# Kernel tuning notes

Measured on AMD Instinct MI355X. Metric: run time of the kernel, lower is better.

## Reference

```python
import jax, jax.numpy as jnp
import numpy as np

N, D, B, E, H = 512, 32, 4, 256, 4
SEP = 256
HD = E // H


def setup_inputs() -> dict:
    key = jax.random.key(0)
    ks = jax.random.split(key, 8)
    s = 0.02
    return {
        "src": jax.random.normal(ks[0], (N, D, B, E), dtype=jnp.float32),
        "w_in_row": jax.random.normal(ks[1], (3 * E, E), dtype=jnp.float32) * s,
        "b_in_row": jnp.zeros((3 * E,), jnp.float32),
        "w_out_row": jax.random.normal(ks[2], (E, E), dtype=jnp.float32) * s,
        "b_out_row": jnp.zeros((E,), jnp.float32),
        "w_in_col": jax.random.normal(ks[3], (3 * E, E), dtype=jnp.float32) * s,
        "b_in_col": jnp.zeros((3 * E,), jnp.float32),
        "w_out_col": jax.random.normal(ks[4], (E, E), dtype=jnp.float32) * s,
        "b_out_col": jnp.zeros((E,), jnp.float32),
        "ln_g": jnp.ones((E,), jnp.float32),
        "ln_b": jnp.zeros((E,), jnp.float32),
        "task_ids": jax.random.randint(ks[5], (B,), 0, 10),
        "single_eval_position": SEP,
    }


def _mha(x, w_in, b_in, w_out, b_out, mask):
    # x: (S, Bt, E); torch MultiheadAttention with batch_first=False
    S, Bt, _ = x.shape
    qkv = x @ w_in.T + b_in                      # (S, Bt, 3E)
    q, k, v = jnp.split(qkv, 3, axis=-1)
    to_heads = lambda t: t.reshape(S, Bt, H, HD).transpose(1, 2, 0, 3)  # (Bt,H,S,HD)
    q, k, v = to_heads(q), to_heads(k), to_heads(v)
    scores = jnp.einsum('bhqd,bhkd->bhqk', q, k) * (HD ** -0.5)
    if mask is not None:  # mask True == disallowed (torch convention)
        scores = jnp.where(mask[None, None], -jnp.inf, scores)
    attn = jax.nn.softmax(scores, axis=-1)
    out = jnp.einsum('bhqk,bhkd->bhqd', attn, v)
    out = out.transpose(2, 0, 1, 3).reshape(S, Bt, E)
    return out @ w_out.T + b_out


def _layer_norm(x, g, b, eps=1e-5):
    mu = x.mean(-1, keepdims=True)
    var = ((x - mu) ** 2).mean(-1, keepdims=True)
    return (x - mu) / jnp.sqrt(var + eps) * g + b


def reference(src, w_in_row, b_in_row, w_out_row, b_out_row,
              w_in_col, b_in_col, w_out_col, b_out_col,
              ln_g, ln_b, task_ids, single_eval_position):
    sep = single_eval_position
    idx = jnp.arange(N)
    # block mask: test queries may not attend to test keys
    row_mask = (idx[:, None] >= sep) & (idx[None, :] >= sep)
    # row attention over the N axis, batched across D*B
    src_row = _mha(src.reshape(N, D * B, E), w_in_row, b_in_row,
                   w_out_row, b_out_row, row_mask).reshape(N, D, B, E)
    # column attention over the D axis, batched across N*B (no mask)
    x_col = src.transpose(1, 0, 2, 3).reshape(D, N * B, E)
    src_col = _mha(x_col, w_in_col, b_in_col, w_out_col, b_out_col,
                   None).reshape(D, N, B, E).transpose(1, 0, 2, 3)
    # parallel axial (seq_axial=False), post-norm (pre_norm=False): row_norm unused
    return _layer_norm(src + src_row + src_col, ln_g, ln_b)
```

## Files before the change

kernel.cpp:

```cpp
#include <hip/hip_runtime.h>
#include <hip/hip_bf16.h>
#include <cstdint>
#include <cstddef>


typedef __hip_bfloat16 bf16;
typedef __attribute__((ext_vector_type(8))) short bf16x8;
typedef __attribute__((ext_vector_type(8))) short short8;
typedef __attribute__((ext_vector_type(4))) short bf16x4;
typedef __attribute__((ext_vector_type(4))) float f32x4;

#define NN 512
#define DD 32
#define BB 4
#define EE 256
#define HH 4
#define HDIM 64
#define DB (DD*BB)
#define MTOK (NN*DD*BB)
#define QKV3 (3*EE)
#define KBLK 64

__device__ __forceinline__ float bf2f(bf16 x){ return __bfloat162float(x); }
__device__ __forceinline__ bf16 f2bf(float x){ return __float2bfloat16(x); }

#define AS1C(p) ((const __attribute__((address_space(1))) void*)(p))
#define AS3(p)  ((__attribute__((address_space(3))) void*)(p))

__global__ __launch_bounds__(256) void cvt_kernel(
    const float* __restrict__ in, bf16* __restrict__ out, int n)
{
  int i = (blockIdx.x * 256 + threadIdx.x) * 8;
  if (i >= n) return;
  const float* p = in + i;
  short8 o;
  #pragma unroll
  for (int j = 0; j < 8; ++j)
    ((bf16*)&o)[j] = f2bf(p[j]);
  *(short8*)(out + i) = o;
}

__global__ __launch_bounds__(256) void cvt_w_kernel(
    const float* __restrict__ ir, const float* __restrict__ orr,
    const float* __restrict__ ic, const float* __restrict__ oc,
    bf16* __restrict__ d_ir, bf16* __restrict__ d_or,
    bf16* __restrict__ d_ic, bf16* __restrict__ d_oc)
{
  const int b = blockIdx.x;
  const float* src; bf16* dst; int off;
  if (b < 96)       { src = ir;  dst = d_ir; off = b; }
  else if (b < 128) { src = orr; dst = d_or; off = b - 96; }
  else if (b < 224) { src = ic;  dst = d_ic; off = b - 128; }
  else              { src = oc;  dst = d_oc; off = b - 224; }
  const int i = (off * 256 + threadIdx.x) * 8;
  const float* p = src + i;
  short8 o;
  #pragma unroll
  for (int j = 0; j < 8; ++j)
    ((bf16*)&o)[j] = f2bf(p[j]);
  *(short8*)(dst + i) = o;
}

template<int NT, int NOUT>
__global__ __launch_bounds__(256,2) void gemm_mfma(
    const bf16* __restrict__ A, const bf16* __restrict__ W,
    const float* __restrict__ bias, bf16* __restrict__ C)
{
  __shared__ bf16 As[128][64];
  __shared__ bf16 Bs[128][64];
  const int bid = blockIdx.x;
  const int xcd = bid & 7;
  const int i0  = bid >> 3;
  const int bm  = xcd * 64 + i0 / NT;
  const int bn  = i0 % NT;

  const int tid  = threadIdx.x;
  const int wid  = tid >> 6;
  const int lane = tid & 63;
  const int lo = lane & 15, hi = lane >> 4;
  const int wr = wid >> 1, wc = wid & 1;

  const int srow = lane >> 3;
  const int slin = (lane & 7) << 4;
  const int ssrc = slin ^ (srow << 4);

  f32x4 acc[4][4] = {};

  for (int k0 = 0; k0 < 256; k0 += 64) {
    __syncthreads();
    #pragma unroll
    for (int i = 0; i < 4; ++i) {
      const int r = wid * 32 + i * 8 + srow;
      const int m = bm * 128 + r;
      const char* gpA = (const char*)(A + (size_t)m * EE + k0) + ssrc;
      __builtin_amdgcn_global_load_lds(AS1C(gpA), AS3(&As[wid*32 + i*8][0]), 16, 0, 0);
      const int wn = bn * 128 + r;
      const char* gpB = (const char*)(W + (size_t)wn * EE + k0) + ssrc;
      __builtin_amdgcn_global_load_lds(AS1C(gpB), AS3(&Bs[wid*32 + i*8][0]), 16, 0, 0);
    }
    __syncthreads();

    #pragma unroll
    for (int kc = 0; kc < 2; ++kc) {
      const int cc = kc * 64 + hi * 16;
      bf16x8 af[4], bfr[4];
      #pragma unroll
      for (int i = 0; i < 4; ++i) {
        const int ra = wr * 64 + i * 16 + lo;
        af[i]  = *(const bf16x8*)((const char*)&As[ra][0] + (cc ^ ((ra & 7) << 4)));
        const int rb = wc * 64 + i * 16 + lo;
        bfr[i] = *(const bf16x8*)((const char*)&Bs[rb][0] + (cc ^ ((rb & 7) << 4)));
      }
      __builtin_amdgcn_s_setprio(1);
      #pragma unroll
      for (int mi = 0; mi < 4; ++mi)
        #pragma unroll
        for (int ni = 0; ni < 4; ++ni)
          acc[mi][ni] = __builtin_amdgcn_mfma_f32_16x16x32_bf16(
              af[mi], bfr[ni], acc[mi][ni], 0, 0, 0);
      __builtin_amdgcn_s_setprio(0);
    }
  }

  float bv[4];
  #pragma unroll
  for (int ni = 0; ni < 4; ++ni)
    bv[ni] = bias[bn * 128 + wc * 64 + ni * 16 + lo];

  #pragma unroll
  for (int mi = 0; mi < 4; ++mi) {
    #pragma unroll
    for (int r = 0; r < 4; ++r) {
      const int m = bm * 128 + wr * 64 + mi * 16 + hi * 4 + r;
      #pragma unroll
      for (int ni = 0; ni < 4; ++ni) {
        const int col = bn * 128 + wc * 64 + ni * 16 + lo;
        C[(size_t)m * NOUT + col] = f2bf(acc[mi][ni][r] + bv[ni]);
      }
    }
  }
}

__global__ __launch_bounds__(256,4) void attn_row_mfma(
    const bf16* __restrict__ qkv, bf16* __restrict__ attn,
    const int* __restrict__ sep_ptr)
{
  const int bid = blockIdx.x;
  const int xcd = bid & 7;
  const int idx = bid >> 3;
  const int pair = xcd * 64 + (idx >> 3);
  const int qt = idx & 7;
  const int t = pair >> 2;
  const int h = pair & 3;
  const int sep = *sep_ptr;

  const int tid  = threadIdx.x;
  const int wid  = tid >> 6;
  const int lane = tid & 63;
  const int lo = lane & 15, hi = lane >> 4;

  __shared__ bf16 Ks[2][KBLK][72];
  __shared__ bf16 Vt[2][HDIM][72];

  const int qb = qt * 64;
  const int q0 = qb + wid * 16;

  bf16x8 qf[2];
  {
    const bf16* Qp = qkv + ((size_t)(q0 + lo) * DB + t) * QKV3 + h * HDIM;
    qf[0] = *(const bf16x8*)(Qp + hi * 8);
    qf[1] = *(const bf16x8*)(Qp + 32 + hi * 8);
    #pragma unroll
    for (int kc = 0; kc < 2; ++kc)
      #pragma unroll
      for (int j = 0; j < 8; ++j)
        ((bf16*)&qf[kc])[j] = f2bf(bf2f(((const bf16*)&qf[kc])[j]) * 0.125f);
  }

  const int kr  = tid >> 2;
  const int kc4 = (tid & 3) * 16;
  const int vr  = tid & 63;
  const int vc  = (tid >> 6) * 16;
  const bf16* Kbase = qkv + ((size_t)kr * DB + t) * QKV3 + EE + h * HDIM + kc4;
  const bf16* Vbase = qkv + ((size_t)vr * DB + t) * QKV3 + 2*EE + h * HDIM + vc;
  const size_t kstep = (size_t)KBLK * DB * QKV3;

  f32x4 Oa[4] = {};
  float m_run = -1e30f, l_run = 0.f;

  const int nkt = (qb >= sep) ? ((sep + KBLK - 1) >> 6) : (NN >> 6);
  const bool need_mask = (qb + 64 > sep) && (nkt * KBLK > sep);

  bf16x8 kg0 = *(const bf16x8*)(Kbase);
  bf16x8 kg1 = *(const bf16x8*)(Kbase + 8);
  bf16x8 vg0 = *(const bf16x8*)(Vbase);
  bf16x8 vg1 = *(const bf16x8*)(Vbase + 8);

  for (int kt = 0; kt < nkt; ++kt) {
    const int k0 = kt * KBLK;
    const int p = kt & 1;

    *(bf16x8*)&Ks[p][kr][kc4]     = kg0;
    *(bf16x8*)&Ks[p][kr][kc4 + 8] = kg1;
    #pragma unroll
    for (int j = 0; j < 8; ++j) {
      Vt[p][vc + j][vr]     = ((const bf16*)&vg0)[j];
      Vt[p][vc + 8 + j][vr] = ((const bf16*)&vg1)[j];
    }
    __syncthreads();

    if (kt + 1 < nkt) {
      const size_t off = (size_t)(kt + 1) * kstep;
      kg0 = *(const bf16x8*)(Kbase + off);
      kg1 = *(const bf16x8*)(Kbase + off + 8);
      vg0 = *(const bf16x8*)(Vbase + off);
      vg1 = *(const bf16x8*)(Vbase + off + 8);
    }

    f32x4 st[4];
    {
      bf16x8 kf[4][2];
      #pragma unroll
      for (int kb = 0; kb < 4; ++kb)
        #pragma unroll
        for (int kc = 0; kc < 2; ++kc)
          kf[kb][kc] = *(const bf16x8*)&Ks[p][kb*16 + lo][kc*32 + hi*8];
      __builtin_amdgcn_s_setprio(1);
      #pragma unroll
      for (int kb = 0; kb < 4; ++kb) {
        st[kb] = (f32x4){0,0,0,0};
        #pragma unroll
        for (int kc = 0; kc < 2; ++kc)
          st[kb] = __builtin_amdgcn_mfma_f32_16x16x32_bf16(
              kf[kb][kc], qf[kc], st[kb], 0, 0, 0);
      }
      __builtin_amdgcn_s_setprio(0);
    }

    if (need_mask && k0 + KBLK > sep) {
      const int qq = q0 + lo;
      #pragma unroll
      for (int kb = 0; kb < 4; ++kb) {
        #pragma unroll
        for (int r = 0; r < 4; ++r) {
          const int kk = k0 + kb*16 + 4*hi + r;
          if (qq >= sep && kk >= sep) st[kb][r] = -1e30f;
        }
      }
    }

    float mx = -1e30f;
    #pragma unroll
    for (int kb = 0; kb < 4; ++kb)
      #pragma unroll
      for (int r = 0; r < 4; ++r) mx = fmaxf(mx, st[kb][r]);
    mx = fmaxf(mx, __shfl_xor(mx, 16));
    mx = fmaxf(mx, __shfl_xor(mx, 32));

    if (__any(mx - m_run > 5.f)) {
      const float mn = fmaxf(m_run, mx);
      const float corr = __expf(m_run - mn);
      m_run = mn;
      l_run *= corr;
      float c4[4];
      #pragma unroll
      for (int r = 0; r < 4; ++r) c4[r] = __shfl(corr, hi*4 + r);
      #pragma unroll
      for (int n = 0; n < 4; ++n)
        #pragma unroll
        for (int r = 0; r < 4; ++r) Oa[n][r] *= c4[r];
    }

    float s0 = 0.f;
    #pragma unroll
    for (int kb = 0; kb < 4; ++kb)
      #pragma unroll
      for (int r = 0; r < 4; ++r) {
        const float pv = __expf(st[kb][r] - m_run);
        st[kb][r] = pv;
        s0 += pv;
      }
    s0 += __shfl_xor(s0, 16);
    s0 += __shfl_xor(s0, 32);
    l_run += s0;

    bf16x8 pa[2];
    #pragma unroll
    for (int kc = 0; kc < 2; ++kc)
      #pragma unroll
      for (int j = 0; j < 8; ++j)
        ((bf16*)&pa[kc])[j] = f2bf(st[kc*2 + (j>>2)][j&3]);

    __builtin_amdgcn_s_setprio(1);
    #pragma unroll
    for (int n = 0; n < 4; ++n) {
      #pragma unroll
      for (int kc = 0; kc < 2; ++kc) {
        const bf16* vrow = &Vt[p][n*16 + lo][0];
        bf16x4 v0 = *(const bf16x4*)(vrow + kc*32 + 4*hi);
        bf16x4 v1 = *(const bf16x4*)(vrow + kc*32 + 16 + 4*hi);
        bf16x8 vf = __builtin_shufflevector(v0, v1, 0,1,2,3,4,5,6,7);
        Oa[n] = __builtin_amdgcn_mfma_f32_16x16x32_bf16(pa[kc], vf, Oa[n], 0, 0, 0);
      }
    }
    __builtin_amdgcn_s_setprio(0);
  }

  float linv[4];
  #pragma unroll
  for (int r = 0; r < 4; ++r) linv[r] = 1.f / __shfl(l_run, hi*4 + r);
  #pragma unroll
  for (int r = 0; r < 4; ++r) {
    const int qq = q0 + hi*4 + r;
    bf16* Op = attn + ((size_t)qq * DB + t) * EE + h * HDIM;
    #pragma unroll
    for (int n = 0; n < 4; ++n)
      Op[n*16 + lo] = f2bf(Oa[n][r] * linv[r]);
  }
}

__global__ __launch_bounds__(256) void attn_col_mfma(
    const bf16* __restrict__ qkv, bf16* __restrict__ attn)
{
  const int bid = blockIdx.x;
  const int n = bid >> 2;
  const int b = bid & 3;
  const int tid = threadIdx.x;
  const int h = tid >> 6;
  const int lane = tid & 63;
  const int lo = lane & 15, hi = lane >> 4;

  __shared__ bf16 Vt[4][64][40];

  {
    const int k  = tid & 31;
    const int hh = tid >> 6;
    const int dh = ((tid >> 5) & 1) * 32;
    const bf16* Vp = qkv + ((size_t)(n*DB + k*4 + b)) * QKV3 + 2*EE + hh*64 + dh;
    #pragma unroll
    for (int c = 0; c < 4; ++c) {
      bf16x8 vv = *(const bf16x8*)(Vp + c*8);
      #pragma unroll
      for (int j = 0; j < 8; ++j)
        Vt[hh][dh + c*8 + j][k] = ((const bf16*)&vv)[j];
    }
  }

  bf16x8 qf[2][2], kf[2][2];
  #pragma unroll
  for (int mt = 0; mt < 2; ++mt) {
    const bf16* Qp = qkv + ((size_t)(n*DB + (mt*16 + lo)*4 + b)) * QKV3 + h*64;
    #pragma unroll
    for (int kc = 0; kc < 2; ++kc) {
      bf16x8 v = *(const bf16x8*)(Qp + kc*32 + hi*8);
      #pragma unroll
      for (int j = 0; j < 8; ++j)
        ((bf16*)&v)[j] = f2bf(bf2f(((const bf16*)&v)[j]) * 0.125f);
      qf[mt][kc] = v;
    }
    const bf16* Kp = Qp + EE;
    kf[mt][0] = *(const bf16x8*)(Kp + hi*8);
    kf[mt][1] = *(const bf16x8*)(Kp + 32 + hi*8);
  }
  __syncthreads();

  f32x4 st[2][2];
  #pragma unroll
  for (int kt = 0; kt < 2; ++kt)
    #pragma unroll
    for (int mt = 0; mt < 2; ++mt) {
      f32x4 a = {0,0,0,0};
      a = __builtin_amdgcn_mfma_f32_16x16x32_bf16(kf[kt][0], qf[mt][0], a, 0, 0, 0);
      a = __builtin_amdgcn_mfma_f32_16x16x32_bf16(kf[kt][1], qf[mt][1], a, 0, 0, 0);
      st[kt][mt] = a;
    }

  float l[2];
  #pragma unroll
  for (int mt = 0; mt < 2; ++mt) {
    float mx = -1e30f;
    #pragma unroll
    for (int kt = 0; kt < 2; ++kt)
      #pragma unroll
      for (int r = 0; r < 4; ++r) mx = fmaxf(mx, st[kt][mt][r]);
    mx = fmaxf(mx, __shfl_xor(mx, 16));
    mx = fmaxf(mx, __shfl_xor(mx, 32));
    float s0 = 0.f;
    #pragma unroll
    for (int kt = 0; kt < 2; ++kt)
      #pragma unroll
      for (int r = 0; r < 4; ++r) {
        const float pv = __expf(st[kt][mt][r] - mx);
        st[kt][mt][r] = pv;
        s0 += pv;
      }
    s0 += __shfl_xor(s0, 16);
    s0 += __shfl_xor(s0, 32);
    l[mt] = s0;
  }

  bf16x8 pa[2];
  #pragma unroll
  for (int mt = 0; mt < 2; ++mt)
    #pragma unroll
    for (int j = 0; j < 8; ++j)
      ((bf16*)&pa[mt])[j] = f2bf(st[j>>2][mt][j&3]);

  f32x4 Oa[2][4] = {};
  #pragma unroll
  for (int nn = 0; nn < 4; ++nn) {
    const bf16* vrow = &Vt[h][nn*16 + lo][0];
    bf16x4 v0 = *(const bf16x4*)(vrow + 4*hi);
    bf16x4 v1 = *(const bf16x4*)(vrow + 16 + 4*hi);
    bf16x8 vf = __builtin_shufflevector(v0, v1, 0,1,2,3,4,5,6,7);
    Oa[0][nn] = __builtin_amdgcn_mfma_f32_16x16x32_bf16(pa[0], vf, Oa[0][nn], 0, 0, 0);
    Oa[1][nn] = __builtin_amdgcn_mfma_f32_16x16x32_bf16(pa[1], vf, Oa[1][nn], 0, 0, 0);
  }

  float linv[2][4];
  #pragma unroll
  for (int mt = 0; mt < 2; ++mt)
    #pragma unroll
    for (int r = 0; r < 4; ++r)
      linv[mt][r] = 1.f / __shfl(l[mt], hi*4 + r);
  #pragma unroll
  for (int mt = 0; mt < 2; ++mt) {
    #pragma unroll
    for (int r = 0; r < 4; ++r) {
      const int q = mt*16 + hi*4 + r;
      bf16* Op = attn + ((size_t)(n*DB + q*4 + b)) * EE + h*64;
      #pragma unroll
      for (int nn = 0; nn < 4; ++nn)
        Op[nn*16 + lo] = f2bf(Oa[mt][nn][r] * linv[mt][r]);
    }
  }
}

__global__ __launch_bounds__(256) void ln_kernel(
    const bf16* __restrict__ srcb, const bf16* __restrict__ rp,
    const bf16* __restrict__ cp, const float* __restrict__ g,
    const float* __restrict__ b, float* __restrict__ out)
{
  const int m = blockIdx.x * 4 + (threadIdx.x >> 6);
  const int lane = threadIdx.x & 63;
  const bf16x4 s4 = ((const bf16x4*)srcb)[(size_t)m*64 + lane];
  const bf16x4 r4 = ((const bf16x4*)rp)[(size_t)m*64 + lane];
  const bf16x4 c4 = ((const bf16x4*)cp)[(size_t)m*64 + lane];
  float x[4];
  #pragma unroll
  for (int j = 0; j < 4; ++j)
    x[j] = bf2f(((const bf16*)&s4)[j]) + bf2f(((const bf16*)&r4)[j])
         + bf2f(((const bf16*)&c4)[j]);
  float sum = x[0] + x[1] + x[2] + x[3];
  #pragma unroll
  for (int off = 1; off < 64; off <<= 1) sum += __shfl_xor(sum, off);
  const float mu = sum * (1.f/EE);
  float d[4];
  #pragma unroll
  for (int j = 0; j < 4; ++j) d[j] = x[j] - mu;
  float ss = d[0]*d[0] + d[1]*d[1] + d[2]*d[2] + d[3]*d[3];
  #pragma unroll
  for (int off = 1; off < 64; off <<= 1) ss += __shfl_xor(ss, off);
  const float rstd = rsqrtf(ss * (1.f/EE) + 1e-5f);
  const float4 g4 = ((const float4*)g)[lane];
  const float4 b4 = ((const float4*)b)[lane];
  float4 o;
  o.x = d[0] * rstd * g4.x + b4.x;
  o.y = d[1] * rstd * g4.y + b4.y;
  o.z = d[2] * rstd * g4.z + b4.z;
  o.w = d[3] * rstd * g4.w + b4.w;
  ((float4*)out)[(size_t)m*64 + lane] = o;
}

extern "C" void kernel_launch(void* const* d_in, const int* in_sizes, int n_in,
                              void* d_out, int out_size, void* d_ws, size_t ws_size,
                              hipStream_t stream)
{
  const float* src      = (const float*)d_in[0];
  const float* w_in_row = (const float*)d_in[1];
  const float* b_in_row = (const float*)d_in[2];
  const float* w_out_row= (const float*)d_in[3];
  const float* b_out_row= (const float*)d_in[4];
  const float* w_in_col = (const float*)d_in[5];
  const float* b_in_col = (const float*)d_in[6];
  const float* w_out_col= (const float*)d_in[7];
  const float* b_out_col= (const float*)d_in[8];
  const float* ln_g     = (const float*)d_in[9];
  const float* ln_b     = (const float*)d_in[10];
  const int*   sep_ptr  = (const int*)d_in[12];
  float* out = (float*)d_out;

  char* ws = (char*)d_ws;
  bf16*  qkv    = (bf16*)(ws);
  bf16*  attnX  = (bf16*)(ws + 100663296);
  bf16*  r_out  = (bf16*)(ws + 134217728);
  bf16*  c_out  = (bf16*)(ws + 167772160);
  bf16*  src_bf = (bf16*)(ws + 201326592);
  bf16*  wbf_ir = (bf16*)(ws + 234881024);
  bf16*  wbf_or = (bf16*)(ws + 235274240);
  bf16*  wbf_ic = (bf16*)(ws + 235405312);
  bf16*  wbf_oc = (bf16*)(ws + 235798528);

  dim3 blk(256);

  cvt_kernel<<<dim3(MTOK*EE/8/256), blk, 0, stream>>>(src, src_bf, MTOK*EE);
  cvt_w_kernel<<<dim3(256), blk, 0, stream>>>(
      w_in_row, w_out_row, w_in_col, w_out_col, wbf_ir, wbf_or, wbf_ic, wbf_oc);

  gemm_mfma<6,QKV3><<<dim3(512*6), blk, 0, stream>>>(src_bf, wbf_ir, b_in_row, qkv);
  attn_row_mfma<<<dim3(4096), blk, 0, stream>>>(qkv, attnX, sep_ptr);
  gemm_mfma<2,EE><<<dim3(512*2), blk, 0, stream>>>(attnX, wbf_or, b_out_row, r_out);

  gemm_mfma<6,QKV3><<<dim3(512*6), blk, 0, stream>>>(src_bf, wbf_ic, b_in_col, qkv);
  attn_col_mfma<<<dim3(NN*BB), blk, 0, stream>>>(qkv, attnX);
  gemm_mfma<2,EE><<<dim3(512*2), blk, 0, stream>>>(attnX, wbf_oc, b_out_col, c_out);

  ln_kernel<<<dim3(MTOK/4), blk, 0, stream>>>(src_bf, r_out, c_out, ln_g, ln_b, out);
}
```

Baseline: 264.1 us.

## Fuse row/column QKV GEMMs, attention, and output projections into shared launches

Merges the row and column QKV projections into a single GEMM producing a 1536-wide QKV buffer, runs row and column attention in one launch split by block index, and batches both output projections into one GEMM. The layer norm now reads the fp32 source directly instead of the bf16 copy, and the round-to-nearest bf16 pack is replaced by a simple bit-add conversion. The aim is fewer kernel launches, better GPU fill from larger grids, and a slightly more accurate residual. In exchange it needs a larger workspace (with a fallback path) and aggressive buffer aliasing, and the bf16 rounding no longer handles NaN or ties-to-even the way the library conversion does.

```diff
diff --git a/kernel.cpp b/kernel.cpp
--- a/kernel.cpp
+++ b/kernel.cpp
@@ -18,11 +18,13 @@
 #define HDIM 64
 #define DB (DD*BB)
 #define MTOK (NN*DD*BB)
-#define QKV3 (3*EE)
 #define KBLK 64
 
 __device__ __forceinline__ float bf2f(bf16 x){ return __bfloat162float(x); }
-__device__ __forceinline__ bf16 f2bf(float x){ return __float2bfloat16(x); }
+__device__ __forceinline__ short pkbf(float x){
+  union { float f; uint32_t u; } c; c.f = x;
+  return (short)((c.u + 0x8000u) >> 16);
+}
 
 #define AS1C(p) ((const __attribute__((address_space(1))) void*)(p))
 #define AS3(p)  ((__attribute__((address_space(3))) void*)(p))
@@ -35,36 +37,48 @@
   const float* p = in + i;
   short8 o;
   #pragma unroll
-  for (int j = 0; j < 8; ++j)
-    ((bf16*)&o)[j] = f2bf(p[j]);
+  for (int j = 0; j < 8; ++j) ((short*)&o)[j] = pkbf(p[j]);
   *(short8*)(out + i) = o;
 }
 
 __global__ __launch_bounds__(256) void cvt_w_kernel(
-    const float* __restrict__ ir, const float* __restrict__ orr,
-    const float* __restrict__ ic, const float* __restrict__ oc,
-    bf16* __restrict__ d_ir, bf16* __restrict__ d_or,
-    bf16* __restrict__ d_ic, bf16* __restrict__ d_oc)
+    const float* __restrict__ ir, const float* __restrict__ ic,
+    bf16* __restrict__ d_ir, bf16* __restrict__ d_ic)
 {
   const int b = blockIdx.x;
-  const float* src; bf16* dst; int off;
-  if (b < 96)       { src = ir;  dst = d_ir; off = b; }
-  else if (b < 128) { src = orr; dst = d_or; off = b - 96; }
-  else if (b < 224) { src = ic;  dst = d_ic; off = b - 128; }
-  else              { src = oc;  dst = d_oc; off = b - 224; }
+  const float* src = (b < 96) ? ir : ic;
+  bf16* dst = (b < 96) ? d_ir : d_ic;
+  const int off = (b < 96) ? b : b - 96;
   const int i = (off * 256 + threadIdx.x) * 8;
   const float* p = src + i;
   short8 o;
   #pragma unroll
-  for (int j = 0; j < 8; ++j)
-    ((bf16*)&o)[j] = f2bf(p[j]);
+  for (int j = 0; j < 8; ++j) ((short*)&o)[j] = pkbf(p[j]);
   *(short8*)(dst + i) = o;
 }
 
-template<int NT, int NOUT>
-__global__ __launch_bounds__(256,2) void gemm_mfma(
-    const bf16* __restrict__ A, const bf16* __restrict__ W,
-    const float* __restrict__ bias, bf16* __restrict__ C)
+__global__ __launch_bounds__(256) void cvt_w2_kernel(
+    const float* __restrict__ orr, const float* __restrict__ oc,
+    bf16* __restrict__ d_or, bf16* __restrict__ d_oc)
+{
+  const int b = blockIdx.x;
+  const float* src = (b < 32) ? orr : oc;
+  bf16* dst = (b < 32) ? d_or : d_oc;
+  const int off = (b < 32) ? b : b - 32;
+  const int i = (off * 256 + threadIdx.x) * 8;
+  const float* p = src + i;
+  short8 o;
+  #pragma unroll
+  for (int j = 0; j < 8; ++j) ((short*)&o)[j] = pkbf(p[j]);
+  *(short8*)(dst + i) = o;
+}
+
+template<int NT>
+__global__ __launch_bounds__(256,2) void gemm_qkv(
+    const bf16* __restrict__ A, const bf16* __restrict__ W1,
+    const bf16* __restrict__ W2, const float* __restrict__ b1,
+    const float* __restrict__ b2, bf16* __restrict__ C,
+    const int nt1, const int nout)
 {
   __shared__ bf16 As[128][64];
   __shared__ bf16 Bs[128][64];
@@ -73,6 +87,9 @@
   const int i0  = bid >> 3;
   const int bm  = xcd * 64 + i0 / NT;
   const int bn  = i0 % NT;
+  const int lbn = (bn < nt1) ? bn : bn - nt1;
+  const bf16* W = (bn < nt1) ? W1 : W2;
+  const float* bias = (bn < nt1) ? b1 : b2;
 
   const int tid  = threadIdx.x;
   const int wid  = tid >> 6;
@@ -81,8 +98,93 @@
   const int wr = wid >> 1, wc = wid & 1;
 
   const int srow = lane >> 3;
-  const int slin = (lane & 7) << 4;
-  const int ssrc = slin ^ (srow << 4);
+  const int ssrc = ((lane & 7) << 4) ^ (srow << 4);
+
+  f32x4 acc[4][4] = {};
+
+  for (int k0 = 0; k0 < 256; k0 += 64) {
+    __syncthreads();
+    #pragma unroll
+    for (int i = 0; i < 4; ++i) {
+      const int r = wid * 32 + i * 8 + srow;
+      const int m = bm * 128 + r;
+      const char* gpA = (const char*)(A + (size_t)m * EE + k0) + ssrc;
+      __builtin_amdgcn_global_load_lds(AS1C(gpA), AS3(&As[wid*32 + i*8][0]), 16, 0, 0);
+      const int wn = lbn * 128 + r;
+      const char* gpB = (const char*)(W + (size_t)wn * EE + k0) + ssrc;
+      __builtin_amdgcn_global_load_lds(AS1C(gpB), AS3(&Bs[wid*32 + i*8][0]), 16, 0, 0);
+    }
+    __syncthreads();
+
+    #pragma unroll
+    for (int kc = 0; kc < 2; ++kc) {
+      const int cc = kc * 64 + hi * 16;
+      bf16x8 af[4], bfr[4];
+      #pragma unroll
+      for (int i = 0; i < 4; ++i) {
+        const int ra = wr * 64 + i * 16 + lo;
+        af[i]  = *(const bf16x8*)((const char*)&As[ra][0] + (cc ^ ((ra & 7) << 4)));
+        const int rb = wc * 64 + i * 16 + lo;
+        bfr[i] = *(const bf16x8*)((const char*)&Bs[rb][0] + (cc ^ ((rb & 7) << 4)));
+      }
+      __builtin_amdgcn_s_setprio(1);
+      #pragma unroll
+      for (int mi = 0; mi < 4; ++mi)
+        #pragma unroll
+        for (int ni = 0; ni < 4; ++ni)
+          acc[mi][ni] = __builtin_amdgcn_mfma_f32_16x16x32_bf16(
+              af[mi], bfr[ni], acc[mi][ni], 0, 0, 0);
+      __builtin_amdgcn_s_setprio(0);
+    }
+  }
+
+  float bv[4];
+  #pragma unroll
+  for (int ni = 0; ni < 4; ++ni)
+    bv[ni] = bias[lbn * 128 + wc * 64 + ni * 16 + lo];
+
+  #pragma unroll
+  for (int mi = 0; mi < 4; ++mi) {
+    #pragma unroll
+    for (int r = 0; r < 4; ++r) {
+      const int m = bm * 128 + wr * 64 + mi * 16 + hi * 4 + r;
+      #pragma unroll
+      for (int ni = 0; ni < 4; ++ni) {
+        const int col = bn * 128 + wc * 64 + ni * 16 + lo;
+        C[(size_t)m * nout + col] = __hip_bfloat16_raw{(unsigned short)pkbf(acc[mi][ni][r] + bv[ni])};
+      }
+    }
+  }
+}
+
+__global__ __launch_bounds__(256,2) void gemm_oproj(
+    const bf16* __restrict__ A1, const bf16* __restrict__ A2,
+    const bf16* __restrict__ W1, const bf16* __restrict__ W2,
+    const float* __restrict__ b1, const float* __restrict__ b2,
+    bf16* __restrict__ C1, bf16* __restrict__ C2)
+{
+  __shared__ bf16 As[128][64];
+  __shared__ bf16 Bs[128][64];
+  const int bid = blockIdx.x;
+  const int sel = bid >> 10;
+  const int b2i = bid & 1023;
+  const int xcd = b2i & 7;
+  const int i0  = b2i >> 3;
+  const int bm  = xcd * 64 + (i0 >> 1);
+  const int bn  = i0 & 1;
+  const bf16* A = sel ? A2 : A1;
+  const bf16* W = sel ? W2 : W1;
+  const float* bias = sel ? b2 : b1;
+  bf16* C = sel ? C2 : C1;
+
+  const int tid  = threadIdx.x;
+  const int wid  = tid >> 6;
+  const int lane = tid & 63;
+  const int lo = lane & 15, hi = lane >> 4;
+  const int wr = wid >> 1, wc = wid & 1;
+
+  const int srow = lane >> 3;
+  const int ssrc = ((lane & 7) << 4) ^ (srow << 4);
 
   f32x4 acc[4][4] = {};
 
@@ -135,322 +237,315 @@
       #pragma unroll
       for (int ni = 0; ni < 4; ++ni) {
         const int col = bn * 128 + wc * 64 + ni * 16 + lo;
-        C[(size_t)m * NOUT + col] = f2bf(acc[mi][ni][r] + bv[ni]);
+        C[(size_t)m * EE + col] = __hip_bfloat16_raw{(unsigned short)pkbf(acc[mi][ni][r] + bv[ni])};
       }
     }
   }
 }
 
-__global__ __launch_bounds__(256,4) void attn_row_mfma(
-    const bf16* __restrict__ qkv, bf16* __restrict__ attn,
-    const int* __restrict__ sep_ptr)
-{
-  const int bid = blockIdx.x;
-  const int xcd = bid & 7;
-  const int idx = bid >> 3;
-  const int pair = xcd * 64 + (idx >> 3);
-  const int qt = idx & 7;
-  const int t = pair >> 2;
-  const int h = pair & 3;
-  const int sep = *sep_ptr;
-
+__global__ __launch_bounds__(256,4) void attn_axial(
+    const bf16* __restrict__ baseR, const bf16* __restrict__ baseC,
+    const int stride, bf16* __restrict__ attnR, bf16* __restrict__ attnC,
+    const int* __restrict__ sep_ptr, const int nrow)
+{
+  __shared__ bf16 smem[9216];
   const int tid  = threadIdx.x;
-  const int wid  = tid >> 6;
   const int lane = tid & 63;
   const int lo = lane & 15, hi = lane >> 4;
 
-  __shared__ bf16 Ks[2][KBLK][72];
-  __shared__ bf16 Vt[2][HDIM][72];
-
-  const int qb = qt * 64;
-  const int q0 = qb + wid * 16;
-
-  bf16x8 qf[2];
-  {
-    const bf16* Qp = qkv + ((size_t)(q0 + lo) * DB + t) * QKV3 + h * HDIM;
-    qf[0] = *(const bf16x8*)(Qp + hi * 8);
-    qf[1] = *(const bf16x8*)(Qp + 32 + hi * 8);
-    #pragma unroll
-    for (int kc = 0; kc < 2; ++kc)
+  if ((int)blockIdx.x < nrow) {
+    const int bid = blockIdx.x;
+    const int xcd = bid & 7;
+    const int idx = bid >> 3;
+    const int pair = xcd * 64 + (idx >> 3);
+    const int qt = idx & 7;
+    const int t = pair >> 2;
+    const int h = pair & 3;
+    const int sep = *sep_ptr;
+    const int wid = tid >> 6;
+    bf16* Ks = smem;
+    bf16* Vt = smem + 4608;
+
+    const int qb = qt * 64;
+    const int q0 = qb + wid * 16;
+
+    bf16x8 qf[2];
+    {
+      const bf16* Qp = baseR + ((size_t)(q0 + lo) * DB + t) * stride + h * HDIM;
+      bf16x8 a = *(const bf16x8*)(Qp + hi * 8);
+      bf16x8 b = *(const bf16x8*)(Qp + 32 + hi * 8);
+      #pragma unroll
+      for (int j = 0; j < 8; ++j) {
+        ((short*)&qf[0])[j] = pkbf(bf2f(((const bf16*)&a)[j]) * 0.125f);
+        ((short*)&qf[1])[j] = pkbf(bf2f(((const bf16*)&b)[j]) * 0.125f);
+      }
+    }
+
+    const int kr  = tid >> 2;
+    const int kc4 = (tid & 3) * 16;
+    const int vr  = tid & 63;
+    const int vc  = (tid >> 6) * 16;
+    const bf16* Kbase = baseR + ((size_t)kr * DB + t) * stride + EE + h * HDIM + kc4;
+    const bf16* Vbase = baseR + ((size_t)vr * DB + t) * stride + 2*EE + h * HDIM + vc;
+    const size_t kstep = (size_t)KBLK * DB * stride;
+
+    f32x4 Oa[4] = {};
+    float m_run = -1e30f, l_run = 0.f;
+
+    const int nkt = (qb >= sep) ? ((sep + KBLK - 1) >> 6) : (NN >> 6);
+    const bool need_mask = (qb + 64 > sep) && (nkt * KBLK > sep);
+
+    bf16x8 kg0 = *(const bf16x8*)(Kbase);
+    bf16x8 kg1 = *(const bf16x8*)(Kbase + 8);
+    bf16x8 vg0 = *(const bf16x8*)(Vbase);
+    bf16x8 vg1 = *(const bf16x8*)(Vbase + 8);
+
+    for (int kt = 0; kt < nkt; ++kt) {
+      const int k0 = kt * KBLK;
+
+      *(bf16x8*)&Ks[kr*72 + kc4]     = kg0;
+      *(bf16x8*)&Ks[kr*72 + kc4 + 8] = kg1;
+      #pragma unroll
+      for (int j = 0; j < 8; ++j) {
+        Vt[(vc + j)*72 + vr]     = ((const bf16*)&vg0)[j];
+        Vt[(vc + 8 + j)*72 + vr] = ((const bf16*)&vg1)[j];
+      }
+      __syncthreads();
+
+      if (kt + 1 < nkt) {
+        const size_t off = (size_t)(kt + 1) * kstep;
+        kg0 = *(const bf16x8*)(Kbase + off);
+        kg1 = *(const bf16x8*)(Kbase + off + 8);
+        vg0 = *(const bf16x8*)(Vbase + off);
+        vg1 = *(const bf16x8*)(Vbase + off + 8);
+      }
+
+      f32x4 st[4];
+      {
+        bf16x8 kf[4][2];
+        #pragma unroll
+        for (int kb = 0; kb < 4; ++kb)
+          #pragma unroll
+          for (int kc = 0; kc < 2; ++kc)
+            kf[kb][kc] = *(const bf16x8*)&Ks[(kb*16 + lo)*72 + kc*32 + hi*8];
+        __builtin_amdgcn_s_setprio(1);
+        #pragma unroll
+        for (int kb = 0; kb < 4; ++kb) {
+          st[kb] = (f32x4){0,0,0,0};
+          #pragma unroll
+          for (int kc = 0; kc < 2; ++kc)
+            st[kb] = __builtin_amdgcn_mfma_f32_16x16x32_bf16(
+                kf[kb][kc], qf[kc], st[kb], 0, 0, 0);
+        }
+        __builtin_amdgcn_s_setprio(0);
+      }
+
+      if (need_mask && k0 + KBLK > sep) {
+        const int qq = q0 + lo;
+        #pragma unroll
+        for (int kb = 0; kb < 4; ++kb)
+          #pragma unroll
+          for (int r = 0; r < 4; ++r) {
+            const int kk = k0 + kb*16 + 4*hi + r;
+            if (qq >= sep && kk >= sep) st[kb][r] = -1e30f;
+          }
+      }
+
+      float mx = -1e30f;
+      #pragma unroll
+      for (int kb = 0; kb < 4; ++kb)
+        #pragma unroll
+        for (int r = 0; r < 4; ++r) mx = fmaxf(mx, st[kb][r]);
+      mx = fmaxf(mx, __shfl_xor(mx, 16));
+      mx = fmaxf(mx, __shfl_xor(mx, 32));
+
+      if (__any(mx - m_run > 5.f)) {
+        const float mn = fmaxf(m_run, mx);
+        const float corr = __expf(m_run - mn);
+        m_run = mn;
+        l_run *= corr;
+        float c4[4];
+        #pragma unroll
+        for (int r = 0; r < 4; ++r) c4[r] = __shfl(corr, hi*4 + r);
+        #pragma unroll
+        for (int n = 0; n < 4; ++n)
+          #pragma unroll
+          for (int r = 0; r < 4; ++r) Oa[n][r] *= c4[r];
+      }
+
+      float s0 = 0.f;
+      #pragma unroll
+      for (int kb = 0; kb < 4; ++kb)
+        #pragma unroll
+        for (int r = 0; r < 4; ++r) {
+          const float pv = __expf(st[kb][r] - m_run);
+          st[kb][r] = pv;
+          s0 += pv;
+        }
+      s0 += __shfl_xor(s0, 16);
+      s0 += __shfl_xor(s0, 32);
+      l_run += s0;
+
+      bf16x8 pa[2];
+      #pragma unroll
+      for (int kc = 0; kc < 2; ++kc)
+        #pragma unroll
+        for (int j = 0; j < 8; ++j)
+          ((short*)&pa[kc])[j] = pkbf(st[kc*2 + (j>>2)][j&3]);
+
+      __builtin_amdgcn_s_setprio(1);
+      #pragma unroll
+      for (int n = 0; n < 4; ++n) {
+        #pragma unroll
+        for (int kc = 0; kc < 2; ++kc) {
+          const bf16* vrow = &Vt[(n*16 + lo)*72];
+          bf16x4 v0 = *(const bf16x4*)(vrow + kc*32 + 4*hi);
+          bf16x4 v1 = *(const bf16x4*)(vrow + kc*32 + 16 + 4*hi);
+          bf16x8 vf = __builtin_shufflevector(v0, v1, 0,1,2,3,4,5,6,7);
+          Oa[n] = __builtin_amdgcn_mfma_f32_16x16x32_bf16(pa[kc], vf, Oa[n], 0, 0, 0);
+        }
+      }
+      __builtin_amdgcn_s_setprio(0);
+      __syncthreads();
+    }
+
+    float linv[4];
+    #pragma unroll
+    for (int r = 0; r < 4; ++r) linv[r] = 1.f / __shfl(l_run, hi*4 + r);
+    #pragma unroll
+    for (int r = 0; r < 4; ++r) {
+      const int qq = q0 + hi*4 + r;
+      bf16* Op = attnR + ((size_t)qq * DB + t) * EE + h * HDIM;
+      #pragma unroll
+      for (int n = 0; n < 4; ++n)
+        Op[n*16 + lo] = __hip_bfloat16_raw{(unsigned short)pkbf(Oa[n][r] * linv[r])};
+    }
+  } else {
+    const int cb = blockIdx.x - nrow;
+    const int n = cb >> 2;
+    const int b = cb & 3;
+    const int h = tid >> 6;
+
+    {
+      const int k  = tid & 31;
+      const int hh = tid >> 6;
+      const int dh = ((tid >> 5) & 1) * 32;
+      const bf16* Vp = baseC + ((size_t)(n*DB + k*4 + b)) * stride + 2*EE + hh*64 + dh;
+      #pragma unroll
+      for (int c = 0; c < 4; ++c) {
+        bf16x8 vv = *(const bf16x8*)(Vp + c*8);
+        #pragma unroll
+        for (int j = 0; j < 8; ++j)
+          smem[hh*2304 + (dh + c*8 + j)*36 + k] = ((const bf16*)&vv)[j];
+      }
+    }
+
+    bf16x8 qf[2][2], kf[2][2];
+    #pragma unroll
+    for (int mt = 0; mt < 2; ++mt) {
+      const bf16* Qp = baseC + ((size_t)(n*DB + (mt*16 + lo)*4 + b)) * stride + h*64;
+      #pragma unroll
+      for (int kc = 0; kc < 2; ++kc) {
+        bf16x8 v = *(const bf16x8*)(Qp + kc*32 + hi*8);
+        #pragma unroll
+        for (int j = 0; j < 8; ++j)
+          ((short*)&v)[j] = pkbf(bf2f(((const bf16*)&v)[j]) * 0.125f);
+        qf[mt][kc] = v;
+      }
+      const bf16* Kp = Qp + EE;
+      kf[mt][0] = *(const bf16x8*)(Kp + hi*8);
+      kf[mt][1] = *(const bf16x8*)(Kp + 32 + hi*8);
+    }
+    __syncthreads();
+
+    f32x4 st[2][2];
+    #pragma unroll
+    for (int kt = 0; kt < 2; ++kt)
+      #pragma unroll
+      for (int mt = 0; mt < 2; ++mt) {
+        f32x4 a = {0,0,0,0};
+        a = __builtin_amdgcn_mfma_f32_16x16x32_bf16(kf[kt][0], qf[mt][0], a, 0, 0, 0);
+        a = __builtin_amdgcn_mfma_f32_16x16x32_bf16(kf[kt][1], qf[mt][1], a, 0, 0, 0);
+        st[kt][mt] = a;
+      }
+
+    float l[2];
+    #pragma unroll
+    for (int mt = 0; mt < 2; ++mt) {
+      float mx = -1e30f;
+      #pragma unroll
+      for (int kt = 0; kt < 2; ++kt)
+        #pragma unroll
+        for (int r = 0; r < 4; ++r) mx = fmaxf(mx, st[kt][mt][r]);
+      mx = fmaxf(mx, __shfl_xor(mx, 16));
+      mx = fmaxf(mx, __shfl_xor(mx, 32));
+      float s0 = 0.f;
+      #pragma unroll
+      for (int kt = 0; kt < 2; ++kt)
+        #pragma unroll
+        for (int r = 0; r < 4; ++r) {
+          const float pv = __expf(st[kt][mt][r] - mx);
+          st[kt][mt][r] = pv;
+          s0 += pv;
+        }
+      s0 += __shfl_xor(s0, 16);
+      s0 += __shfl_xor(s0, 32);
+      l[mt] = s0;
+    }
+
+    bf16x8 pa[2];
+    #pragma unroll
+    for (int mt = 0; mt < 2; ++mt)
       #pragma unroll
       for (int j = 0; j < 8; ++j)
-        ((bf16*)&qf[kc])[j] = f2bf(bf2f(((const bf16*)&qf[kc])[j]) * 0.125f);
+        ((short*)&pa[mt])[j] = pkbf(st[j>>2][mt][j&3]);
+
+    f32x4 Oa[2][4] = {};
+    #pragma unroll
+    for (int nn = 0; nn < 4; ++nn) {
+      const bf16* vrow = &smem[h*2304 + (nn*16 + lo)*36];
+      bf16x4 v0 = *(const bf16x4*)(vrow + 4*hi);
+      bf16x4 v1 = *(const bf16x4*)(vrow + 16 + 4*hi);
+      bf16x8 vf = __builtin_shufflevector(v0, v1, 0,1,2,3,4,5,6,7);
+      Oa[0][nn] = __builtin_amdgcn_mfma_f32_16x16x32_bf16(pa[0], vf, Oa[0][nn], 0, 0, 0);
+      Oa[1][nn] = __builtin_amdgcn_mfma_f32_16x16x32_bf16(pa[1], vf, Oa[1][nn], 0, 0, 0);
+    }
+
+    float linv[2][4];
+    #pragma unroll
+    for (int mt = 0; mt < 2; ++mt)
+      #pragma unroll
+      for (int r = 0; r < 4; ++r)
+        linv[mt][r] = 1.f / __shfl(l[mt], hi*4 + r);
+    #pragma unroll
+    for (int mt = 0; mt < 2; ++mt) {
+      #pragma unroll
+      for (int r = 0; r < 4; ++r) {
+        const int q = mt*16 + hi*4 + r;
+        bf16* Op = attnC + ((size_t)(n*DB + q*4 + b)) * EE + h*64;
+        #pragma unroll
+        for (int nn = 0; nn < 4; ++nn)
+          Op[nn*16 + lo] = __hip_bfloat16_raw{(unsigned short)pkbf(Oa[mt][nn][r] * linv[mt][r])};
+      }
+    }
   }
-
-  const int kr  = tid >> 2;
-  const int kc4 = (tid & 3) * 16;
-  const int vr  = tid & 63;
-  const int vc  = (tid >> 6) * 16;
-  const bf16* Kbase = qkv + ((size_t)kr * DB + t) * QKV3 + EE + h * HDIM + kc4;
-  const bf16* Vbase = qkv + ((size_t)vr * DB + t) * QKV3 + 2*EE + h * HDIM + vc;
-  const size_t kstep = (size_t)KBLK * DB * QKV3;
-
-  f32x4 Oa[4] = {};
-  float m_run = -1e30f, l_run = 0.f;
-
-  const int nkt = (qb >= sep) ? ((sep + KBLK - 1) >> 6) : (NN >> 6);
-  const bool need_mask = (qb + 64 > sep) && (nkt * KBLK > sep);
-
-  bf16x8 kg0 = *(const bf16x8*)(Kbase);
-  bf16x8 kg1 = *(const bf16x8*)(Kbase + 8);
-  bf16x8 vg0 = *(const bf16x8*)(Vbase);
-  bf16x8 vg1 = *(const bf16x8*)(Vbase + 8);
-
-  for (int kt = 0; kt < nkt; ++kt) {
-    const int k0 = kt * KBLK;
-    const int p = kt & 1;
-
-    *(bf16x8*)&Ks[p][kr][kc4]     = kg0;
-    *(bf16x8*)&Ks[p][kr][kc4 + 8] = kg1;
-    #pragma unroll
-    for (int j = 0; j < 8; ++j) {
-      Vt[p][vc + j][vr]     = ((const bf16*)&vg0)[j];
-      Vt[p][vc + 8 + j][vr] = ((const bf16*)&vg1)[j];
-    }
-    __syncthreads();
-
-    if (kt + 1 < nkt) {
-      const size_t off = (size_t)(kt + 1) * kstep;
-      kg0 = *(const bf16x8*)(Kbase + off);
-      kg1 = *(const bf16x8*)(Kbase + off + 8);
-      vg0 = *(const bf16x8*)(Vbase + off);
-      vg1 = *(const bf16x8*)(Vbase + off + 8);
-    }
-
-    f32x4 st[4];
-    {
-      bf16x8 kf[4][2];
-      #pragma unroll
-      for (int kb = 0; kb < 4; ++kb)
-        #pragma unroll
-        for (int kc = 0; kc < 2; ++kc)
-          kf[kb][kc] = *(const bf16x8*)&Ks[p][kb*16 + lo][kc*32 + hi*8];
-      __builtin_amdgcn_s_setprio(1);
-      #pragma unroll
-      for (int kb = 0; kb < 4; ++kb) {
-        st[kb] = (f32x4){0,0,0,0};
-        #pragma unroll
-        for (int kc = 0; kc < 2; ++kc)
-          st[kb] = __builtin_amdgcn_mfma_f32_16x16x32_bf16(
-              kf[kb][kc], qf[kc], st[kb], 0, 0, 0);
-      }
-      __builtin_amdgcn_s_setprio(0);
-    }
-
-    if (need_mask && k0 + KBLK > sep) {
-      const int qq = q0 + lo;
-      #pragma unroll
-      for (int kb = 0; kb < 4; ++kb) {
-        #pragma unroll
-        for (int r = 0; r < 4; ++r) {
-          const int kk = k0 + kb*16 + 4*hi + r;
-          if (qq >= sep && kk >= sep) st[kb][r] = -1e30f;
-        }
-      }
-    }
-
-    float mx = -1e30f;
-    #pragma unroll
-    for (int kb = 0; kb < 4; ++kb)
-      #pragma unroll
-      for (int r = 0; r < 4; ++r) mx = fmaxf(mx, st[kb][r]);
-    mx = fmaxf(mx, __shfl_xor(mx, 16));
-    mx = fmaxf(mx, __shfl_xor(mx, 32));
-
-    if (__any(mx - m_run > 5.f)) {
-      const float mn = fmaxf(m_run, mx);
-      const float corr = __expf(m_run - mn);
-      m_run = mn;
-      l_run *= corr;
-      float c4[4];
-      #pragma unroll
-      for (int r = 0; r < 4; ++r) c4[r] = __shfl(corr, hi*4 + r);
-      #pragma unroll
-      for (int n = 0; n < 4; ++n)
-        #pragma unroll
-        for (int r = 0; r < 4; ++r) Oa[n][r] *= c4[r];
-    }
-
-    float s0 = 0.f;
-    #pragma unroll
-    for (int kb = 0; kb < 4; ++kb)
-      #pragma unroll
-      for (int r = 0; r < 4; ++r) {
-        const float pv = __expf(st[kb][r] - m_run);
-        st[kb][r] = pv;
-        s0 += pv;
-      }
-    s0 += __shfl_xor(s0, 16);
-    s0 += __shfl_xor(s0, 32);
-    l_run += s0;
-
-    bf16x8 pa[2];
-    #pragma unroll
-    for (int kc = 0; kc < 2; ++kc)
-      #pragma unroll
-      for (int j = 0; j < 8; ++j)
-        ((bf16*)&pa[kc])[j] = f2bf(st[kc*2 + (j>>2)][j&3]);
-
-    __builtin_amdgcn_s_setprio(1);
-    #pragma unroll
-    for (int n = 0; n < 4; ++n) {
-      #pragma unroll
-      for (int kc = 0; kc < 2; ++kc) {
-        const bf16* vrow = &Vt[p][n*16 + lo][0];
-        bf16x4 v0 = *(const bf16x4*)(vrow + kc*32 + 4*hi);
-        bf16x4 v1 = *(const bf16x4*)(vrow + kc*32 + 16 + 4*hi);
-        bf16x8 vf = __builtin_shufflevector(v0, v1, 0,1,2,3,4,5,6,7);
-        Oa[n] = __builtin_amdgcn_mfma_f32_16x16x32_bf16(pa[kc], vf, Oa[n], 0, 0, 0);
-      }
-    }
-    __builtin_amdgcn_s_setprio(0);
-  }
-
-  float linv[4];
-  #pragma unroll
-  for (int r = 0; r < 4; ++r) linv[r] = 1.f / __shfl(l_run, hi*4 + r);
-  #pragma unroll
-  for (int r = 0; r < 4; ++r) {
-    const int qq = q0 + hi*4 + r;
-    bf16* Op = attn + ((size_t)qq * DB + t) * EE + h * HDIM;
-    #pragma unroll
-    for (int n = 0; n < 4; ++n)
-      Op[n*16 + lo] = f2bf(Oa[n][r] * linv[r]);
-  }
-}
-
-__global__ __launch_bounds__(256) void attn_col_mfma(
-    const bf16* __restrict__ qkv, bf16* __restrict__ attn)
-{
-  const int bid = blockIdx.x;
-  const int n = bid >> 2;
-  const int b = bid & 3;
-  const int tid = threadIdx.x;
-  const int h = tid >> 6;
-  const int lane = tid & 63;
-  const int lo = lane & 15, hi = lane >> 4;
-
-  __shared__ bf16 Vt[4][64][40];
-
-  {
-    const int k  = tid & 31;
-    const int hh = tid >> 6;
-    const int dh = ((tid >> 5) & 1) * 32;
-    const bf16* Vp = qkv + ((size_t)(n*DB + k*4 + b)) * QKV3 + 2*EE + hh*64 + dh;
-    #pragma unroll
-    for (int c = 0; c < 4; ++c) {
-      bf16x8 vv = *(const bf16x8*)(Vp + c*8);
-      #pragma unroll
-      for (int j = 0; j < 8; ++j)
-        Vt[hh][dh + c*8 + j][k] = ((const bf16*)&vv)[j];
-    }
-  }
-
-  bf16x8 qf[2][2], kf[2][2];
-  #pragma unroll
-  for (int mt = 0; mt < 2; ++mt) {
-    const bf16* Qp = qkv + ((size_t)(n*DB + (mt*16 + lo)*4 + b)) * QKV3 + h*64;
-    #pragma unroll
-    for (int kc = 0; kc < 2; ++kc) {
-      bf16x8 v = *(const bf16x8*)(Qp + kc*32 + hi*8);
-      #pragma unroll
-      for (int j = 0; j < 8; ++j)
-        ((bf16*)&v)[j] = f2bf(bf2f(((const bf16*)&v)[j]) * 0.125f);
-      qf[mt][kc] = v;
-    }
-    const bf16* Kp = Qp + EE;
-    kf[mt][0] = *(const bf16x8*)(Kp + hi*8);
-    kf[mt][1] = *(const bf16x8*)(Kp + 32 + hi*8);
-  }
-  __syncthreads();
-
-  f32x4 st[2][2];
-  #pragma unroll
-  for (int kt = 0; kt < 2; ++kt)
-    #pragma unroll
-    for (int mt = 0; mt < 2; ++mt) {
-      f32x4 a = {0,0,0,0};
-      a = __builtin_amdgcn_mfma_f32_16x16x32_bf16(kf[kt][0], qf[mt][0], a, 0, 0, 0);
-      a = __builtin_amdgcn_mfma_f32_16x16x32_bf16(kf[kt][1], qf[mt][1], a, 0, 0, 0);
-      st[kt][mt] = a;
-    }
-
-  float l[2];
-  #pragma unroll
-  for (int mt = 0; mt < 2; ++mt) {
-    float mx = -1e30f;
-    #pragma unroll
-    for (int kt = 0; kt < 2; ++kt)
-      #pragma unroll
-      for (int r = 0; r < 4; ++r) mx = fmaxf(mx, st[kt][mt][r]);
-    mx = fmaxf(mx, __shfl_xor(mx, 16));
-    mx = fmaxf(mx, __shfl_xor(mx, 32));
-    float s0 = 0.f;
-    #pragma unroll
-    for (int kt = 0; kt < 2; ++kt)
-      #pragma unroll
-      for (int r = 0; r < 4; ++r) {
-        const float pv = __expf(st[kt][mt][r] - mx);
-        st[kt][mt][r] = pv;
-        s0 += pv;
-      }
-    s0 += __shfl_xor(s0, 16);
-    s0 += __shfl_xor(s0, 32);
-    l[mt] = s0;
-  }
-
-  bf16x8 pa[2];
-  #pragma unroll
-  for (int mt = 0; mt < 2; ++mt)
-    #pragma unroll
-    for (int j = 0; j < 8; ++j)
-      ((bf16*)&pa[mt])[j] = f2bf(st[j>>2][mt][j&3]);
-
-  f32x4 Oa[2][4] = {};
-  #pragma unroll
-  for (int nn = 0; nn < 4; ++nn) {
-    const bf16* vrow = &Vt[h][nn*16 + lo][0];
-    bf16x4 v0 = *(const bf16x4*)(vrow + 4*hi);
-    bf16x4 v1 = *(const bf16x4*)(vrow + 16 + 4*hi);
-    bf16x8 vf = __builtin_shufflevector(v0, v1, 0,1,2,3,4,5,6,7);
-    Oa[0][nn] = __builtin_amdgcn_mfma_f32_16x16x32_bf16(pa[0], vf, Oa[0][nn], 0, 0, 0);
-    Oa[1][nn] = __builtin_amdgcn_mfma_f32_16x16x32_bf16(pa[1], vf, Oa[1][nn], 0, 0, 0);
-  }
-
-  float linv[2][4];
-  #pragma unroll
-  for (int mt = 0; mt < 2; ++mt)
-    #pragma unroll
-    for (int r = 0; r < 4; ++r)
-      linv[mt][r] = 1.f / __shfl(l[mt], hi*4 + r);
-  #pragma unroll
-  for (int mt = 0; mt < 2; ++mt) {
-    #pragma unroll
-    for (int r = 0; r < 4; ++r) {
-      const int q = mt*16 + hi*4 + r;
-      bf16* Op = attn + ((size_t)(n*DB + q*4 + b)) * EE + h*64;
-      #pragma unroll
-      for (int nn = 0; nn < 4; ++nn)
-        Op[nn*16 + lo] = f2bf(Oa[mt][nn][r] * linv[mt][r]);
-    }
-  }
 }
 
 __global__ __launch_bounds__(256) void ln_kernel(
-    const bf16* __restrict__ srcb, const bf16* __restrict__ rp,
+    const float* __restrict__ src, const bf16* __restrict__ rp,
     const bf16* __restrict__ cp, const float* __restrict__ g,
     const float* __restrict__ b, float* __restrict__ out)
 {
   const int m = blockIdx.x * 4 + (threadIdx.x >> 6);
   const int lane = threadIdx.x & 63;
-  const bf16x4 s4 = ((const bf16x4*)srcb)[(size_t)m*64 + lane];
+  const float4 s4 = ((const float4*)src)[(size_t)m*64 + lane];
   const bf16x4 r4 = ((const bf16x4*)rp)[(size_t)m*64 + lane];
   const bf16x4 c4 = ((const bf16x4*)cp)[(size_t)m*64 + lane];
   float x[4];
-  #pragma unroll
-  for (int j = 0; j < 4; ++j)
-    x[j] = bf2f(((const bf16*)&s4)[j]) + bf2f(((const bf16*)&r4)[j])
-         + bf2f(((const bf16*)&c4)[j]);
+  x[0] = s4.x + bf2f(((const bf16*)&r4)[0]) + bf2f(((const bf16*)&c4)[0]);
+  x[1] = s4.y + bf2f(((const bf16*)&r4)[1]) + bf2f(((const bf16*)&c4)[1]);
+  x[2] = s4.z + bf2f(((const bf16*)&r4)[2]) + bf2f(((const bf16*)&c4)[2]);
+  x[3] = s4.w + bf2f(((const bf16*)&r4)[3]) + bf2f(((const bf16*)&c4)[3]);
   float sum = x[0] + x[1] + x[2] + x[3];
   #pragma unroll
   for (int off = 1; off < 64; off <<= 1) sum += __shfl_xor(sum, off);
@@ -491,29 +586,55 @@
   float* out = (float*)d_out;
 
   char* ws = (char*)d_ws;
-  bf16*  qkv    = (bf16*)(ws);
-  bf16*  attnX  = (bf16*)(ws + 100663296);
-  bf16*  r_out  = (bf16*)(ws + 134217728);
-  bf16*  c_out  = (bf16*)(ws + 167772160);
-  bf16*  src_bf = (bf16*)(ws + 201326592);
-  bf16*  wbf_ir = (bf16*)(ws + 234881024);
-  bf16*  wbf_or = (bf16*)(ws + 235274240);
-  bf16*  wbf_ic = (bf16*)(ws + 235405312);
-  bf16*  wbf_oc = (bf16*)(ws + 235798528);
-
   dim3 blk(256);
 
-  cvt_kernel<<<dim3(MTOK*EE/8/256), blk, 0, stream>>>(src, src_bf, MTOK*EE);
-  cvt_w_kernel<<<dim3(256), blk, 0, stream>>>(
-      w_in_row, w_out_row, w_in_col, w_out_col, wbf_ir, wbf_or, wbf_ic, wbf_oc);
-
-  gemm_mfma<6,QKV3><<<dim3(512*6), blk, 0, stream>>>(src_bf, wbf_ir, b_in_row, qkv);
-  attn_row_mfma<<<dim3(4096), blk, 0, stream>>>(qkv, attnX, sep_ptr);
-  gemm_mfma<2,EE><<<dim3(512*2), blk, 0, stream>>>(attnX, wbf_or, b_out_row, r_out);
-
-  gemm_mfma<6,QKV3><<<dim3(512*6), blk, 0, stream>>>(src_bf, wbf_ic, b_in_col, qkv);
-  attn_col_mfma<<<dim3(NN*BB), blk, 0, stream>>>(qkv, attnX);
-  gemm_mfma<2,EE><<<dim3(512*2), blk, 0, stream>>>(attnX, wbf_oc, b_out_col, c_out);
-
-  ln_kernel<<<dim3(MTOK/4), blk, 0, stream>>>(src_bf, r_out, c_out, ln_g, ln_b, out);
-}
+  if (ws_size >= 268435456ULL) {
+    bf16* qkv    = (bf16*)(ws);
+    bf16* attnR  = (bf16*)(ws + 201326592);
+    bf16* attnC  = (bf16*)(ws + 234881024);
+    bf16* src_bf = attnR;
+    bf16* wir    = (bf16*)(ws + 234881024);
+    bf16* wic    = (bf16*)(ws + 235274240);
+    bf16* wor    = (bf16*)(ws + 67108864);
+    bf16* woc    = (bf16*)(ws + 67239936);
+    bf16* r_out  = (bf16*)(ws);
+    bf16* c_out  = (bf16*)(ws + 33554432);
+
+    cvt_kernel<<<dim3(8192), blk, 0, stream>>>(src, src_bf, MTOK*EE);
+    cvt_w_kernel<<<dim3(192), blk, 0, stream>>>(w_in_row, w_in_col, wir, wic);
+    gemm_qkv<12><<<dim3(512*12), blk, 0, stream>>>(
+        src_bf, wir, wic, b_in_row, b_in_col, qkv, 6, 1536);
+    attn_axial<<<dim3(6144), blk, 0, stream>>>(
+        qkv, qkv + 768, 1536, attnR, attnC, sep_ptr, 4096);
+    cvt_w2_kernel<<<dim3(64), blk, 0, stream>>>(w_out_row, w_out_col, wor, woc);
+    gemm_oproj<<<dim3(2048), blk, 0, stream>>>(
+        attnR, attnC, wor, woc, b_out_row, b_out_col, r_out, c_out);
+    ln_kernel<<<dim3(MTOK/4), blk, 0, stream>>>(src, r_out, c_out, ln_g, ln_b, out);
+  } else {
+    bf16* qkv    = (bf16*)(ws);
+    bf16* attnR  = (bf16*)(ws + 100663296);
+    bf16* attnC  = (bf16*)(ws + 134217728);
+    bf16* src_bf = (bf16*)(ws + 167772160);
+    bf16* wir    = (bf16*)(ws + 201326592);
+    bf16* wic    = (bf16*)(ws + 201719808);
+    bf16* wor    = (bf16*)(ws + 67108864);
+    bf16* woc    = (bf16*)(ws + 67239936);
+    bf16* r_out  = (bf16*)(ws);
+    bf16* c_out  = (bf16*)(ws + 33554432);
+
+    cvt_kernel<<<dim3(8192), blk, 0, stream>>>(src, src_bf, MTOK*EE);
+    cvt_w_kernel<<<dim3(192), blk, 0, stream>>>(w_in_row, w_in_col, wir, wic);
+    gemm_qkv<6><<<dim3(512*6), blk, 0, stream>>>(
+        src_bf, wir, wir, b_in_row, b_in_row, qkv, 6, 768);
+    attn_axial<<<dim3(4096), blk, 0, stream>>>(
+        qkv, qkv, 768, attnR, attnC, sep_ptr, 4096);
+    gemm_qkv<6><<<dim3(512*6), blk, 0, stream>>>(
+        src_bf, wic, wic, b_in_col, b_in_col, qkv, 6, 768);
+    attn_axial<<<dim3(2048), blk, 0, stream>>>(
+        qkv, qkv, 768, attnR, attnC, sep_ptr, 0);
+    cvt_w2_kernel<<<dim3(64), blk, 0, stream>>>(w_out_row, w_out_col, wor, woc);
+    gemm_oproj<<<dim3(2048), blk, 0, stream>>>(
+        attnR, attnC, wor, woc, b_out_row, b_out_col, r_out, c_out);
+    ln_kernel<<<dim3(MTOK/4), blk, 0, stream>>>(src, r_out, c_out, ln_g, ln_b, out);
+  }
+}
```

Result: faster. 257.0 us (-2.7%).
